# Kernel optimization log

Measured on AMD Instinct MI355X. Metric: run time of the kernel, lower is better.

Reference implementation:

```python
import jax, jax.numpy as jnp
import numpy as np

B, S, H, V, L = 64, 512, 1024, 50257, 1
EPS = 1e-10

def setup_inputs() -> dict:
    key = jax.random.key(0)
    ks = jax.random.split(key, 16)
    inp = {
        "input_seq": jax.random.randint(ks[0], (B,), 0, V),
        "last_context": jax.random.normal(ks[1], (B, H), jnp.float32),
        "h0": jax.random.normal(ks[2], (L, B, H), jnp.float32),
        "c0": jax.random.normal(ks[3], (L, B, H), jnp.float32),
        "encoder_outputs": jax.random.normal(ks[4], (S, B, H), jnp.float32),
        "inp_mask": jnp.ones((S, B), jnp.float32),
        # parameters
        "emb": jax.random.normal(ks[5], (V, H), jnp.float32) * 0.02,
        "W_ih": jax.random.normal(ks[6], (4 * H, H), jnp.float32) / np.sqrt(H),
        "W_hh": jax.random.normal(ks[7], (4 * H, H), jnp.float32) / np.sqrt(H),
        "b_ih": jnp.zeros((4 * H,), jnp.float32),
        "b_hh": jnp.zeros((4 * H,), jnp.float32),
        "W_attn": jax.random.normal(ks[8], (H, 2 * H), jnp.float32) / np.sqrt(2 * H),
        "v_attn": jax.random.normal(ks[9], (H,), jnp.float32) / np.sqrt(H),
        "W_concat": jax.random.normal(ks[10], (H, 2 * H), jnp.float32) / np.sqrt(2 * H),
        "b_concat": jnp.zeros((H,), jnp.float32),
        "W_out": jax.random.normal(ks[11], (V, H), jnp.float32) / np.sqrt(H),
        "b_out": jnp.zeros((V,), jnp.float32),
    }
    return inp


def reference(input_seq, last_context, h0, c0, encoder_outputs, inp_mask,
              emb, W_ih, W_hh, b_ih, b_hh, W_attn, v_attn,
              W_concat, b_concat, W_out, b_out):
    # embedding lookup (dropout is identity in eval mode)
    x = emb[input_seq]                                  # [B,H]
    # single-step single-layer LSTM cell (PyTorch gate order i,f,g,o)
    h_prev, c_prev = h0[-1], c0[-1]                     # [B,H]
    gates = x @ W_ih.T + b_ih + h_prev @ W_hh.T + b_hh  # [B,4H]
    i, f, g, o = jnp.split(gates, 4, axis=-1)
    c_new = jax.nn.sigmoid(f) * c_prev + jax.nn.sigmoid(i) * jnp.tanh(g)
    h_new = jax.nn.sigmoid(o) * jnp.tanh(c_new)         # [B,H] == rnn_output == s_t

    # Luong 'concat' attention (Attention class)
    enc = encoder_outputs.transpose(1, 0, 2)            # [B,S,H]
    Wh, We = W_attn[:, :H], W_attn[:, H:]               # split concat-linear
    energy = jnp.tanh(h_new @ Wh.T[None if False else ...][..., :] if False else
                      jnp.tanh(0))                       # placeholder never used
    energy = jnp.tanh((h_new @ Wh.T)[:, None, :] + jnp.einsum('bsh,gh->bsg', enc, We))  # [B,S,H]
    scores = jnp.einsum('bsh,h->bs', energy, v_attn)    # [B,S]
    # NOTE: original code softmaxes over dim=0 (the BATCH dim) — kept faithfully,
    # then masks and renormalizes over the sequence dim.
    a = jax.nn.softmax(scores, axis=0) * inp_mask.T     # [B,S]
    a = a / (a.sum(axis=1, keepdims=True) + EPS)
    context = jnp.einsum('bs,bsh->bh', a, enc)          # [B,H]

    concat_output = jnp.tanh(
        h_new @ W_concat[:, :H].T + context @ W_concat[:, H:].T + b_concat)  # [B,H]
    output = concat_output @ W_out.T + b_out            # [B,V]
    hidden = (h_new[None], c_new[None])                 # [1,B,H] each
    alpha = a[:, None, :]                               # [B,1,S]
    return (output, context, hidden[0], hidden[1], alpha)
```

## Files before the change

### kernel.cpp

```cpp
#include <hip/hip_runtime.h>
#include <cstdint>

#define Bn 64
#define Hn 1024
#define Sn 512
#define Vn 50257

typedef short short8 __attribute__((ext_vector_type(8)));
typedef float f32x4 __attribute__((ext_vector_type(4)));

__device__ inline float fast_exp2(float x){ return __builtin_amdgcn_exp2f(x); }
__device__ inline float fast_rcp(float x){ return __builtin_amdgcn_rcpf(x); }
__device__ inline float fast_tanh(float x){
  float e = fast_exp2(x * 2.8853900817779268f);
  return 1.0f - 2.0f*fast_rcp(e + 1.0f);
}
__device__ inline float fast_sigmoid(float x){
  return fast_rcp(1.0f + fast_exp2(-1.4426950408889634f*x));
}
__device__ inline unsigned int bf16rne(float f){
  unsigned int u = __float_as_uint(f);
  return (u + 0x7fffu + ((u>>16)&1u)) >> 16;
}
__device__ inline unsigned int bfpack(float lo, float hi){
  return bf16rne(lo) | (bf16rne(hi) << 16);
}

__global__ void prep_kernel(const int* __restrict__ idx, const float4* __restrict__ emb,
                            const float4* __restrict__ h0, float4* __restrict__ xT4,
                            float4* __restrict__ hT4){
  int b = blockIdx.x; int t = threadIdx.x;
  int row = idx[b];
  xT4[t*64 + b] = emb[(long)row*256 + t];
  hT4[t*64 + b] = h0[b*256 + t];
}

__global__ void conv_we_kernel(const float* __restrict__ W_attn, unsigned short* __restrict__ we){
  int id0 = blockIdx.x*1024 + threadIdx.x;
  #pragma unroll
  for (int i=0;i<4;i++){
    int id = id0 + i*256;
    int g = id >> 10, k = id & 1023;
    we[id] = (unsigned short)bf16rne(W_attn[g*2048 + 1024 + k]);
  }
}

__global__ void zero_kernel(float* __restrict__ p, int n){
  int id = blockIdx.x*256 + threadIdx.x;
  if (id < n) p[id] = 0.f;
}

template<int TRB, int NM, bool DOTANH>
__global__ __launch_bounds__(256) void tile_gemm_f32(
    const float4* __restrict__ A0, const float* __restrict__ W0, int w0s,
    const float4* __restrict__ A1, const float* __restrict__ W1, int w1s, int w1o,
    const float* __restrict__ bias0, const float* __restrict__ bias1,
    float* __restrict__ out, int outStride, int K4src)
{
  constexpr int CH_K4 = 16;
  constexpr int CH_F4 = TRB * CH_K4;
  constexpr int LD = CH_F4 / 64;
  __shared__ float4 Wl[4][2][CH_F4];
  __shared__ float red[4][TRB][64];

  int tid = threadIdx.x; int l = tid & 63; int w = tid >> 6;
  int n0 = blockIdx.x * TRB;
  int K4w = K4src >> 2;
  int nch = K4w / CH_K4;
  int k4base = w * K4w;

  float acc[TRB];
  #pragma unroll
  for (int j=0;j<TRB;j++) acc[j]=0.f;

  for (int m=0; m<NM; m++){
    const float*  Wp = (m==0) ? W0 : W1;
    const float4* Ap = (m==0) ? A0 : A1;
    long ws = (m==0) ? w0s : w1s;
    long wo = (m==0) ? 0   : w1o;

    float4 r[LD];
    #pragma unroll
    for (int i=0;i<LD;i++){
      int idx = i*64 + l; int row = idx >> 4; int q = idx & 15;
      r[i] = *(const float4*)(Wp + (long)(n0+row)*ws + wo + (long)k4base*4 + q*4);
    }
    #pragma unroll
    for (int i=0;i<LD;i++){ int idx = i*64 + l; Wl[w][0][idx] = r[i]; }

    for (int c=0; c<nch; c++){
      int cur = c & 1;
      if (c+1 < nch){
        #pragma unroll
        for (int i=0;i<LD;i++){
          int idx = i*64 + l; int row = idx >> 4; int q = idx & 15;
          r[i] = *(const float4*)(Wp + (long)(n0+row)*ws + wo + (long)(k4base + (c+1)*CH_K4)*4 + q*4);
        }
      }
      const float4* wb = &Wl[w][cur][0];
      int k4g = k4base + c*CH_K4;
      #pragma unroll
      for (int kk=0; kk<CH_K4; kk++){
        float4 a = Ap[(long)(k4g+kk)*64 + l];
        #pragma unroll
        for (int j=0;j<TRB;j++){
          float4 wv = wb[j*CH_K4 + kk];
          acc[j] = fmaf(a.x, wv.x, acc[j]);
          acc[j] = fmaf(a.y, wv.y, acc[j]);
          acc[j] = fmaf(a.z, wv.z, acc[j]);
          acc[j] = fmaf(a.w, wv.w, acc[j]);
        }
      }
      if (c+1 < nch){
        #pragma unroll
        for (int i=0;i<LD;i++){ int idx = i*64 + l; Wl[w][cur^1][idx] = r[i]; }
      }
    }
  }

  #pragma unroll
  for (int j=0;j<TRB;j++) red[w][j][l] = acc[j];
  __syncthreads();
  #pragma unroll
  for (int t2=0; t2<(TRB*64)/256; t2++){
    int idx = t2*256 + tid;
    int j  = idx & (TRB-1);
    int l2 = idx / TRB;
    float s = red[0][j][l2] + red[1][j][l2] + red[2][j][l2] + red[3][j][l2];
    int n = n0 + j;
    if (bias0) s += bias0[n];
    if (bias1) s += bias1[n];
    if (DOTANH) s = fast_tanh(s);
    out[(long)l2*outStride + n] = s;
  }
}

__global__ void lstm_kernel(const float* __restrict__ gates, const float* __restrict__ c0,
                            float* __restrict__ h_out, float* __restrict__ c_out,
                            float* __restrict__ hT4){
  int id = blockIdx.x*256 + threadIdx.x;
  int b = id >> 10, h = id & 1023;
  const float* g = gates + (long)b*4096;
  float vi = g[h], vf = g[1024+h], vg = g[2048+h], vo = g[3072+h];
  float cp = c0[id];
  float cn = fast_sigmoid(vf)*cp + fast_sigmoid(vi)*fast_tanh(vg);
  float hn = fast_sigmoid(vo)*fast_tanh(cn);
  c_out[id] = cn; h_out[id] = hn;
  hT4[(h>>2)*256 + b*4 + (h&3)] = hn;
}

__launch_bounds__(256, 2)
__global__ void attn_scores_kernel(const float4* __restrict__ enc, const unsigned short* __restrict__ we,
                                   const float* __restrict__ hWh, const float* __restrict__ vattn,
                                   float* __restrict__ scoresT)
{
  __shared__ unsigned short Asb[64*40];
  __shared__ unsigned short Bsb[256*40];
  int tid = threadIdx.x;
  int bid = blockIdx.x;
  int xcd = bid & 7, slot = bid >> 3;
  int s  = xcd*64 + (slot >> 2);
  int g0 = (slot & 3) * 256;
  int l = tid & 63, w = tid >> 6;
  int quad = l >> 4, l15 = l & 15;

  int arow = tid >> 2, aq = tid & 3;
  long abase = ((long)s*64 + arow)*256;

  f32x4 acc[4][4];
  #pragma unroll
  for (int mt=0;mt<4;mt++)
    #pragma unroll
    for (int gt=0;gt<4;gt++) acc[mt][gt] = 0.f;

  for (int kt=0; kt<32; kt++){
    __syncthreads();
    {
      float4 f0 = enc[abase + kt*8 + aq*2];
      float4 f1 = enc[abase + kt*8 + aq*2 + 1];
      uint4 p;
      p.x = bfpack(f0.x, f0.y); p.y = bfpack(f0.z, f0.w);
      p.z = bfpack(f1.x, f1.y); p.w = bfpack(f1.z, f1.w);
      *(uint4*)&Asb[arow*40 + aq*8] = p;
      #pragma unroll
      for (int p4=0;p4<4;p4++){
        int grow = p4*64 + (tid>>2);
        const uint4* src = (const uint4*)&we[(long)(g0+grow)*1024 + kt*32 + aq*8];
        *(uint4*)&Bsb[grow*40 + aq*8] = *src;
      }
    }
    __syncthreads();
    short8 af[4], bfr[4];
    #pragma unroll
    for (int mt=0;mt<4;mt++) af[mt]  = *(const short8*)&Asb[(mt*16 + l15)*40 + quad*8];
    #pragma unroll
    for (int gt=0;gt<4;gt++) bfr[gt] = *(const short8*)&Bsb[(w*64 + gt*16 + l15)*40 + quad*8];
    #pragma unroll
    for (int mt=0;mt<4;mt++)
      #pragma unroll
      for (int gt=0;gt<4;gt++)
        acc[mt][gt] = __builtin_amdgcn_mfma_f32_16x16x32_bf16(af[mt], bfr[gt], acc[mt][gt], 0,0,0);
  }

  float sp[16];
  #pragma unroll
  for (int i=0;i<16;i++) sp[i]=0.f;
  #pragma unroll
  for (int gt=0;gt<4;gt++){
    int g = g0 + w*64 + gt*16 + l15;
    float vg = vattn[g];
    #pragma unroll
    for (int mt=0;mt<4;mt++){
      #pragma unroll
      for (int r=0;r<4;r++){
        int b = mt*16 + quad*4 + r;
        float val = acc[mt][gt][r] + hWh[b*1024 + g];
        sp[mt*4+r] = fmaf(vg, fast_tanh(val), sp[mt*4+r]);
      }
    }
  }
  #pragma unroll
  for (int off=1; off<16; off<<=1){
    #pragma unroll
    for (int i=0;i<16;i++) sp[i] += __shfl_xor(sp[i], off);
  }
  if (l15 == 0){
    #pragma unroll
    for (int mt=0;mt<4;mt++)
      #pragma unroll
      for (int r=0;r<4;r++){
        int b = mt*16 + quad*4 + r;
        atomicAdd(&scoresT[s*64 + b], sp[mt*4+r]);
      }
  }
}

__launch_bounds__(256, 2)
__global__ void vocab_gemm_kernel(const float* __restrict__ A, const float* __restrict__ W,
                                  const float* __restrict__ bias, float* __restrict__ out)
{
  __shared__ unsigned short Asb[64*40];
  __shared__ unsigned short Bsb[256*40];
  int tid = threadIdx.x;
  int n0 = blockIdx.x * 256;
  int l = tid & 63, w = tid >> 6;
  int quad = l >> 4, l15 = l & 15;

  int arow = tid >> 2, aq = tid & 3;
  int bkq = tid & 7;
  int brow = tid >> 3;

  f32x4 acc[4][4];
  #pragma unroll
  for (int mt=0;mt<4;mt++)
    #pragma unroll
    for (int gt=0;gt<4;gt++) acc[mt][gt] = 0.f;

  for (int kt=0; kt<32; kt++){
    __syncthreads();
    {
      const float4* ap = (const float4*)&A[arow*1024 + kt*32 + aq*8];
      float4 f0 = ap[0], f1 = ap[1];
      uint4 p;
      p.x = bfpack(f0.x, f0.y); p.y = bfpack(f0.z, f0.w);
      p.z = bfpack(f1.x, f1.y); p.w = bfpack(f1.z, f1.w);
      *(uint4*)&Asb[arow*40 + aq*8] = p;
      #pragma unroll
      for (int p4=0;p4<8;p4++){
        int row = p4*32 + brow;
        int gr = n0 + row; if (gr >= Vn) gr = Vn-1;
        float4 f = *(const float4*)&W[(long)gr*1024 + kt*32 + bkq*4];
        uint2 q; q.x = bfpack(f.x, f.y); q.y = bfpack(f.z, f.w);
        *(uint2*)&Bsb[row*40 + bkq*4] = q;
      }
    }
    __syncthreads();
    short8 af[4], bfr[4];
    #pragma unroll
    for (int mt=0;mt<4;mt++) af[mt]  = *(const short8*)&Asb[(mt*16 + l15)*40 + quad*8];
    #pragma unroll
    for (int gt=0;gt<4;gt++) bfr[gt] = *(const short8*)&Bsb[(w*64 + gt*16 + l15)*40 + quad*8];
    #pragma unroll
    for (int mt=0;mt<4;mt++)
      #pragma unroll
      for (int gt=0;gt<4;gt++)
        acc[mt][gt] = __builtin_amdgcn_mfma_f32_16x16x32_bf16(af[mt], bfr[gt], acc[mt][gt], 0,0,0);
  }

  #pragma unroll
  for (int gt=0;gt<4;gt++){
    int n = n0 + w*64 + gt*16 + l15;
    if (n >= Vn) continue;
    float bz = bias[n];
    #pragma unroll
    for (int mt=0;mt<4;mt++){
      #pragma unroll
      for (int r=0;r<4;r++){
        int b = mt*16 + quad*4 + r;
        out[(long)b*Vn + n] = acc[mt][gt][r] + bz;
      }
    }
  }
}

__global__ void softmax_b_kernel(float* __restrict__ a_sb, const float* __restrict__ mask){
  int tid = threadIdx.x; int l = tid & 63; int w = tid >> 6;
  int s = blockIdx.x*4 + w;
  float x = a_sb[s*64 + l];
  float m = x;
  #pragma unroll
  for (int off=1; off<64; off<<=1) m = fmaxf(m, __shfl_xor(m, off));
  float e = fast_exp2((x - m)*1.4426950408889634f);
  float t = e;
  #pragma unroll
  for (int off=1; off<64; off<<=1) t += __shfl_xor(t, off);
  float a = e * fast_rcp(t);
  a *= mask[s*64 + l];
  a_sb[s*64 + l] = a;
}

__global__ void norm_s_kernel(const float* __restrict__ a_sb, float* __restrict__ aBS,
                              float* __restrict__ alpha){
  int b = blockIdx.x; int l = threadIdx.x;
  float tot = 0.f;
  #pragma unroll
  for (int i=0;i<8;i++) tot += a_sb[(l + i*64)*64 + b];
  #pragma unroll
  for (int off=1; off<64; off<<=1) tot += __shfl_xor(tot, off);
  float inv = 1.0f/(tot + 1e-10f);
  #pragma unroll
  for (int i=0;i<8;i++){
    int sidx = l + i*64;
    float v = a_sb[sidx*64 + b]*inv;
    aBS[b*512 + sidx] = v;
    alpha[b*512 + sidx] = v;
  }
}

__global__ void context_kernel(const float* __restrict__ aBS, const float* __restrict__ enc,
                               float* __restrict__ ctx_out, float* __restrict__ ctxT4){
  int h = blockIdx.x*256 + threadIdx.x;
  int b = blockIdx.y;
  const float* ab = aBS + b*512;
  float acc = 0.f;
  for (int s0=0; s0<512; s0+=16){
    float av[16], ev[16];
    #pragma unroll
    for (int i=0;i<16;i++) av[i] = ab[s0+i];
    #pragma unroll
    for (int i=0;i<16;i++) ev[i] = enc[((long)(s0+i)*64 + b)*1024 + h];
    #pragma unroll
    for (int i=0;i<16;i++) acc = fmaf(av[i], ev[i], acc);
  }
  ctx_out[b*1024 + h] = acc;
  ctxT4[(h>>2)*256 + b*4 + (h&3)] = acc;
}

extern "C" void kernel_launch(void* const* d_in, const int* in_sizes, int n_in,
                              void* d_out, int out_size, void* d_ws, size_t ws_size,
                              hipStream_t stream)
{
  const int*   idx    = (const int*)  d_in[0];
  const float* h0     = (const float*)d_in[2];
  const float* c0     = (const float*)d_in[3];
  const float* enc    = (const float*)d_in[4];
  const float* mask   = (const float*)d_in[5];
  const float* emb    = (const float*)d_in[6];
  const float* W_ih   = (const float*)d_in[7];
  const float* W_hh   = (const float*)d_in[8];
  const float* b_ih   = (const float*)d_in[9];
  const float* b_hh   = (const float*)d_in[10];
  const float* W_attn = (const float*)d_in[11];
  const float* v_attn = (const float*)d_in[12];
  const float* W_cat  = (const float*)d_in[13];
  const float* b_cat  = (const float*)d_in[14];
  const float* W_out  = (const float*)d_in[15];
  const float* b_out  = (const float*)d_in[16];

  float* out     = (float*)d_out;
  float* o_ctx   = out + (long)Bn*Vn;
  float* o_h     = o_ctx + Bn*Hn;
  float* o_c     = o_h + Bn*Hn;
  float* o_alpha = o_c + Bn*Hn;

  float* ws    = (float*)d_ws;
  float* xT4   = ws;
  float* hT4   = xT4 + 65536;
  float* gates = hT4 + 65536;
  float* hnT4  = gates + 262144;
  float* hWh   = hnT4 + 65536;
  float* a_sb  = hWh + 65536;
  float* aBS   = a_sb + 32768;
  float* ctxT4 = aBS + 32768;
  float* catRM = ctxT4 + 65536;
  unsigned short* we_bf = (unsigned short*)(catRM + 65536);

  prep_kernel<<<64,256,0,stream>>>(idx, (const float4*)emb, (const float4*)h0,
                                   (float4*)xT4, (float4*)hT4);
  conv_we_kernel<<<1024,256,0,stream>>>(W_attn, we_bf);
  zero_kernel<<<128,256,0,stream>>>(a_sb, 32768);
  tile_gemm_f32<4,2,false><<<1024,256,0,stream>>>((const float4*)xT4, W_ih, 1024,
      (const float4*)hT4, W_hh, 1024, 0, b_ih, b_hh, gates, 4096, 256);
  lstm_kernel<<<256,256,0,stream>>>(gates, c0, o_h, o_c, hnT4);
  tile_gemm_f32<4,1,false><<<256,256,0,stream>>>((const float4*)hnT4, W_attn, 2048,
      nullptr, nullptr, 0, 0, nullptr, nullptr, hWh, 1024, 256);
  attn_scores_kernel<<<2048,256,0,stream>>>((const float4*)enc, we_bf, hWh, v_attn, a_sb);
  softmax_b_kernel<<<128,256,0,stream>>>(a_sb, mask);
  norm_s_kernel<<<64,64,0,stream>>>(a_sb, aBS, o_alpha);
  context_kernel<<<dim3(4,64),256,0,stream>>>(aBS, enc, o_ctx, ctxT4);
  tile_gemm_f32<4,2,true><<<256,256,0,stream>>>((const float4*)hnT4, W_cat, 2048,
      (const float4*)ctxT4, W_cat, 2048, 1024, b_cat, nullptr, catRM, 1024, 256);
  vocab_gemm_kernel<<<197,256,0,stream>>>(catRM, W_out, b_out, out);
}
```

Baseline: 844.0 us.

## Shrink vocab GEMM N-tile to 64 and double-buffer LDS with register prefetch

The vocab projection GEMM now uses 64-column tiles, giving 786 blocks instead of 197, so the grid fills all compute units of the MI355X. It also double-buffers the shared-memory tiles and prefetches the next K-slice into registers while the MFMAs run on the current one. The aim is better coverage of the memory-bound stream over the 200 MB fp32 W_out. In exchange, the A activations are reloaded and converted four times as often, and each wave does less MFMA work per barrier.

```diff
diff --git a/kernel.cpp b/kernel.cpp
--- a/kernel.cpp
+++ b/kernel.cpp
@@ -235,69 +235,81 @@
   }
 }
 
-__launch_bounds__(256, 2)
-__global__ void vocab_gemm_kernel(const float* __restrict__ A, const float* __restrict__ W,
-                                  const float* __restrict__ bias, float* __restrict__ out)
+__global__ __launch_bounds__(256) void vocab_gemm_kernel(
+    const float* __restrict__ A, const float* __restrict__ W,
+    const float* __restrict__ bias, float* __restrict__ out)
 {
-  __shared__ unsigned short Asb[64*40];
-  __shared__ unsigned short Bsb[256*40];
+  __shared__ unsigned short Asb[2][64*40];
+  __shared__ unsigned short Bsb[2][64*40];
   int tid = threadIdx.x;
-  int n0 = blockIdx.x * 256;
+  int n0 = blockIdx.x * 64;
   int l = tid & 63, w = tid >> 6;
   int quad = l >> 4, l15 = l & 15;
 
   int arow = tid >> 2, aq = tid & 3;
-  int bkq = tid & 7;
-  int brow = tid >> 3;
-
-  f32x4 acc[4][4];
-  #pragma unroll
-  for (int mt=0;mt<4;mt++)
-    #pragma unroll
-    for (int gt=0;gt<4;gt++) acc[mt][gt] = 0.f;
+  int gr = n0 + arow; if (gr >= Vn) gr = Vn-1;
+  const float* arp = A + arow*1024 + aq*8;
+  const float* brp = W + (long)gr*1024 + aq*8;
+
+  f32x4 acc[4];
+  #pragma unroll
+  for (int mt=0;mt<4;mt++) acc[mt] = 0.f;
+
+  float4 a0, a1, b0, b1;
+  a0 = *(const float4*)(arp + 0);
+  a1 = *(const float4*)(arp + 4);
+  b0 = *(const float4*)(brp + 0);
+  b1 = *(const float4*)(brp + 4);
+  {
+    uint4 p;
+    p.x = bfpack(a0.x, a0.y); p.y = bfpack(a0.z, a0.w);
+    p.z = bfpack(a1.x, a1.y); p.w = bfpack(a1.z, a1.w);
+    *(uint4*)&Asb[0][arow*40 + aq*8] = p;
+    uint4 q;
+    q.x = bfpack(b0.x, b0.y); q.y = bfpack(b0.z, b0.w);
+    q.z = bfpack(b1.x, b1.y); q.w = bfpack(b1.z, b1.w);
+    *(uint4*)&Bsb[0][arow*40 + aq*8] = q;
+  }
+  __syncthreads();
 
   for (int kt=0; kt<32; kt++){
+    int cur = kt & 1;
+    if (kt < 31){
+      a0 = *(const float4*)(arp + (kt+1)*32 + 0);
+      a1 = *(const float4*)(arp + (kt+1)*32 + 4);
+      b0 = *(const float4*)(brp + (kt+1)*32 + 0);
+      b1 = *(const float4*)(brp + (kt+1)*32 + 4);
+    }
+    short8 af[4], bf;
+    #pragma unroll
+    for (int mt=0;mt<4;mt++) af[mt] = *(const short8*)&Asb[cur][(mt*16 + l15)*40 + quad*8];
+    bf = *(const short8*)&Bsb[cur][(w*16 + l15)*40 + quad*8];
+    #pragma unroll
+    for (int mt=0;mt<4;mt++)
+      acc[mt] = __builtin_amdgcn_mfma_f32_16x16x32_bf16(af[mt], bf, acc[mt], 0,0,0);
     __syncthreads();
-    {
-      const float4* ap = (const float4*)&A[arow*1024 + kt*32 + aq*8];
-      float4 f0 = ap[0], f1 = ap[1];
+    if (kt < 31){
       uint4 p;
-      p.x = bfpack(f0.x, f0.y); p.y = bfpack(f0.z, f0.w);
-      p.z = bfpack(f1.x, f1.y); p.w = bfpack(f1.z, f1.w);
-      *(uint4*)&Asb[arow*40 + aq*8] = p;
-      #pragma unroll
-      for (int p4=0;p4<8;p4++){
-        int row = p4*32 + brow;
-        int gr = n0 + row; if (gr >= Vn) gr = Vn-1;
-        float4 f = *(const float4*)&W[(long)gr*1024 + kt*32 + bkq*4];
-        uint2 q; q.x = bfpack(f.x, f.y); q.y = bfpack(f.z, f.w);
-        *(uint2*)&Bsb[row*40 + bkq*4] = q;
-      }
-    }
-    __syncthreads();
-    short8 af[4], bfr[4];
-    #pragma unroll
-    for (int mt=0;mt<4;mt++) af[mt]  = *(const short8*)&Asb[(mt*16 + l15)*40 + quad*8];
-    #pragma unroll
-    for (int gt=0;gt<4;gt++) bfr[gt] = *(const short8*)&Bsb[(w*64 + gt*16 + l15)*40 + quad*8];
-    #pragma unroll
-    for (int mt=0;mt<4;mt++)
-      #pragma unroll
-      for (int gt=0;gt<4;gt++)
-        acc[mt][gt] = __builtin_amdgcn_mfma_f32_16x16x32_bf16(af[mt], bfr[gt], acc[mt][gt], 0,0,0);
-  }
-
-  #pragma unroll
-  for (int gt=0;gt<4;gt++){
-    int n = n0 + w*64 + gt*16 + l15;
-    if (n >= Vn) continue;
+      p.x = bfpack(a0.x, a0.y); p.y = bfpack(a0.z, a0.w);
+      p.z = bfpack(a1.x, a1.y); p.w = bfpack(a1.z, a1.w);
+      *(uint4*)&Asb[cur^1][arow*40 + aq*8] = p;
+      uint4 q;
+      q.x = bfpack(b0.x, b0.y); q.y = bfpack(b0.z, b0.w);
+      q.z = bfpack(b1.x, b1.y); q.w = bfpack(b1.z, b1.w);
+      *(uint4*)&Bsb[cur^1][arow*40 + aq*8] = q;
+      __syncthreads();
+    }
+  }
+
+  int n = n0 + w*16 + l15;
+  if (n < Vn){
     float bz = bias[n];
     #pragma unroll
     for (int mt=0;mt<4;mt++){
       #pragma unroll
       for (int r=0;r<4;r++){
         int b = mt*16 + quad*4 + r;
-        out[(long)b*Vn + n] = acc[mt][gt][r] + bz;
+        out[(long)b*Vn + n] = acc[mt][r] + bz;
       }
     }
   }
@@ -410,5 +422,5 @@
   context_kernel<<<dim3(4,64),256,0,stream>>>(aBS, enc, o_ctx, ctxT4);
   tile_gemm_f32<4,2,true><<<256,256,0,stream>>>((const float4*)hnT4, W_cat, 2048,
       (const float4*)ctxT4, W_cat, 2048, 1024, b_cat, nullptr, catRM, 1024, 256);
-  vocab_gemm_kernel<<<197,256,0,stream>>>(catRM, W_out, b_out, out);
-}
+  vocab_gemm_kernel<<<786,256,0,stream>>>(catRM, W_out, b_out, out);
+}
```

Result: faster. 753.8 us (-10.7%).
